# Kernel optimization log

Hardware: AMD Instinct MI355X
Metric: run time of the kernel (lower is better)

Reference implementation:

```python
import jax, jax.numpy as jnp
import numpy as np

MODEL_DIM = 1024
NUM_HEADS = 16
DEPTH = MODEL_DIM // NUM_HEADS


def setup_inputs() -> dict:
    key = jax.random.key(0)
    ks = jax.random.split(key, 9)
    B, S, D = 4, 2048, MODEL_DIM
    scale = 1.0 / np.sqrt(D)
    x = jax.random.normal(ks[0], (B, S, D), dtype=jnp.float32)
    wq = jax.random.normal(ks[1], (D, D), dtype=jnp.float32) * scale
    bq = jnp.zeros((D,), dtype=jnp.float32)
    wk = jax.random.normal(ks[2], (D, D), dtype=jnp.float32) * scale
    bk = jnp.zeros((D,), dtype=jnp.float32)
    wv = jax.random.normal(ks[3], (D, D), dtype=jnp.float32) * scale
    bv = jnp.zeros((D,), dtype=jnp.float32)
    wo = jax.random.normal(ks[4], (D, D), dtype=jnp.float32) * scale
    bo = jnp.zeros((D,), dtype=jnp.float32)
    return {"x": x, "wq": wq, "bq": bq, "wk": wk, "bk": bk,
            "wv": wv, "bv": bv, "wo": wo, "bo": bo}


def reference(x, wq, bq, wk, bk, wv, bv, wo, bo):
    B, S, D = x.shape
    H, dh = NUM_HEADS, DEPTH
    # projections
    q = (x @ wq + bq).reshape(B, S, H, dh).transpose(0, 2, 1, 3)  # [B,H,S,dh]
    k = (x @ wk + bk).reshape(B, S, H, dh).transpose(0, 2, 1, 3)
    v = (x @ wv + bv).reshape(B, S, H, dh).transpose(0, 2, 1, 3)
    # scaled dot-product attention (full score matrix, as in source)
    logits = jnp.einsum('bhqd,bhkd->bhqk', q, k) / jnp.sqrt(jnp.float32(dh))
    attn = jax.nn.softmax(logits, axis=-1)
    out = jnp.einsum('bhqk,bhkd->bhqd', attn, v)  # [B,H,S,dh]
    out = out.transpose(0, 2, 1, 3).reshape(B, S, D)
    return out @ wo + bo
```

## Files before the change

kernel.cpp:

```cpp
#include <hip/hip_runtime.h>
#include <hip/hip_bf16.h>


#define S_LEN 2048
#define DMODEL 1024
#define NH 16
#define DH 64
#define BATCH 4
#define MROWS (BATCH * S_LEN)
#define NELEM_X (MROWS * DMODEL)
#define NELEM_W (DMODEL * DMODEL)
#define NELEM_B DMODEL

typedef short short8 __attribute__((ext_vector_type(8)));
typedef float floatx4 __attribute__((ext_vector_type(4)));

__device__ __forceinline__ float bf2f(unsigned short u) {
    union { unsigned int i; float f; } c; c.i = ((unsigned int)u) << 16; return c.f;
}
__device__ __forceinline__ unsigned int f2bf_pk(float lo, float hi) {
    unsigned int r;
    asm("v_cvt_pk_bf16_f32 %0, %1, %2" : "=v"(r) : "v"(lo), "v"(hi));
    return r;
}
__device__ __forceinline__ void async_copy16(const void* g, void* l) {
    __builtin_amdgcn_global_load_lds(
        (const __attribute__((address_space(1))) unsigned int*)g,
        (__attribute__((address_space(3))) unsigned int*)l, 16, 0, 0);
}

__global__ void sniff_kernel(const unsigned short* __restrict__ x, int* flag) {
    __shared__ int cnt;
    if (threadIdx.x == 0) cnt = 0;
    __syncthreads();
    int c = 0;
    for (int i = threadIdx.x; i < 65536; i += 256) {
        unsigned int e = (x[i] >> 7) & 0xFFu;
        if (e >= 0xC0u) c++;
    }
    atomicAdd(&cnt, c);
    __syncthreads();
    if (threadIdx.x == 0) *flag = (cnt > 64) ? 1 : 0;
}

struct ConvArgs { const void* s[5]; unsigned short* d[5]; int n8[5]; };
__global__ void convert_all(ConvArgs a, const int* __restrict__ flag) {
    const int seg = blockIdx.y;
    const int f = *flag;
    const int n8 = a.n8[seg];
    unsigned short* dst = a.d[seg];
    int i = blockIdx.x * blockDim.x + threadIdx.x;
    const int stride = gridDim.x * blockDim.x;
    if (f) {
        const float4* s4 = (const float4*)a.s[seg];
        for (; i < n8; i += stride) {
            float4 x0 = s4[2 * i], x1 = s4[2 * i + 1];
            uint4 o;
            o.x = f2bf_pk(x0.x, x0.y); o.y = f2bf_pk(x0.z, x0.w);
            o.z = f2bf_pk(x1.x, x1.y); o.w = f2bf_pk(x1.z, x1.w);
            *(uint4*)(dst + (size_t)i * 8) = o;
        }
    } else {
        const uint4* s4 = (const uint4*)a.s[seg];
        for (; i < n8; i += stride) *(uint4*)(dst + (size_t)i * 8) = s4[i];
    }
}

struct TWArgs { const void* s[4]; unsigned short* d[4]; };
__global__ void transpose_w(TWArgs a, const int* __restrict__ flag) {
    __shared__ unsigned int Lt[64 * 33];
    const int z = blockIdx.z;
    const int f = *flag;
    const int k0 = blockIdx.x * 64, n0 = blockIdx.y * 64;
    const int t = threadIdx.x;
    const int c = t & 63, rgrp = t >> 6;

    if (f) {
        const float* W = (const float*)a.s[z];
        #pragma unroll
        for (int s = 0; s < 8; s++) {
            int r0 = rgrp * 16 + 2 * s;
            float v0 = W[(size_t)(k0 + r0) * DMODEL + n0 + c];
            float v1 = W[(size_t)(k0 + r0 + 1) * DMODEL + n0 + c];
            Lt[c * 33 + rgrp * 8 + s] = f2bf_pk(v0, v1);
        }
    } else {
        const unsigned short* W = (const unsigned short*)a.s[z];
        #pragma unroll
        for (int s = 0; s < 8; s++) {
            int r0 = rgrp * 16 + 2 * s;
            unsigned int lo = W[(size_t)(k0 + r0) * DMODEL + n0 + c];
            unsigned int hi = W[(size_t)(k0 + r0 + 1) * DMODEL + n0 + c];
            Lt[c * 33 + rgrp * 8 + s] = lo | (hi << 16);
        }
    }
    __syncthreads();
    const int row = t >> 2, j = t & 3;
    unsigned int* outp = (unsigned int*)(a.d[z] + (size_t)(n0 + row) * DMODEL + k0);
    #pragma unroll
    for (int i = 0; i < 8; i++) outp[j * 8 + i] = Lt[row * 33 + j * 8 + i];
}

__global__ __launch_bounds__(256, 2)
void gemm_bias_kernel(const unsigned short* __restrict__ X,
                      const unsigned short* __restrict__ T0, const unsigned short* __restrict__ B0, void* __restrict__ Y0,
                      const unsigned short* __restrict__ T1, const unsigned short* __restrict__ B1, void* __restrict__ Y1,
                      const unsigned short* __restrict__ T2, const unsigned short* __restrict__ B2, void* __restrict__ Y2,
                      float os0, float os1, float os2,
                      const int* __restrict__ flag, int fp32_out)
{
    const unsigned short* Wt = T0; const unsigned short* Bi = B0; void* Y = Y0;
    float os = os0;
    if (blockIdx.z == 1) { Wt = T1; Bi = B1; Y = Y1; os = os1; }
    else if (blockIdx.z == 2) { Wt = T2; Bi = B2; Y = Y2; os = os2; }
    const int f32o = fp32_out ? (*flag) : 0;

    __shared__ __align__(16) unsigned short As[128 * 32];
    __shared__ __align__(16) unsigned short Bs[128 * 32];

    const int t    = threadIdx.x;
    const int lane = t & 63;
    const int wid  = t >> 6;
    const int quad = lane >> 4;
    const int n16  = lane & 15;
    const int wm   = wid >> 1, wn = wid & 1;

    const int m0 = blockIdx.x * 128;
    const int n0 = blockIdx.y * 128;

    floatx4 acc[4][4];
    #pragma unroll
    for (int i = 0; i < 4; i++)
        #pragma unroll
        for (int j = 0; j < 4; j++) acc[i][j] = (floatx4){0.f, 0.f, 0.f, 0.f};

    const int r = t >> 2, c8 = (t & 3) * 8;

    for (int kb = 0; kb < DMODEL; kb += 32) {
        __syncthreads();
        async_copy16(X  + (size_t)(m0 + r)      * DMODEL + kb + c8, As + r * 32 + c8);
        async_copy16(X  + (size_t)(m0 + 64 + r) * DMODEL + kb + c8, As + (64 + r) * 32 + c8);
        async_copy16(Wt + (size_t)(n0 + r)      * DMODEL + kb + c8, Bs + r * 32 + c8);
        async_copy16(Wt + (size_t)(n0 + 64 + r) * DMODEL + kb + c8, Bs + (64 + r) * 32 + c8);
        __syncthreads();

        short8 af[4], bfr[4];
        #pragma unroll
        for (int mt = 0; mt < 4; mt++)
            af[mt] = *(const short8*)(As + (wm * 64 + mt * 16 + n16) * 32 + quad * 8);
        #pragma unroll
        for (int nt = 0; nt < 4; nt++)
            bfr[nt] = *(const short8*)(Bs + (wn * 64 + nt * 16 + n16) * 32 + quad * 8);
        #pragma unroll
        for (int mt = 0; mt < 4; mt++)
            #pragma unroll
            for (int nt = 0; nt < 4; nt++)
                acc[mt][nt] = __builtin_amdgcn_mfma_f32_16x16x32_bf16(af[mt], bfr[nt], acc[mt][nt], 0, 0, 0);
    }

    float bv4[4];
    #pragma unroll
    for (int nt = 0; nt < 4; nt++) bv4[nt] = bf2f(Bi[n0 + wn * 64 + nt * 16 + n16]) * os;
    #pragma unroll
    for (int mt = 0; mt < 4; mt++)
        #pragma unroll
        for (int rr = 0; rr < 4; rr++) {
            size_t row = (size_t)(m0 + wm * 64 + mt * 16 + quad * 4 + rr);
            if (f32o) {
                #pragma unroll
                for (int nt = 0; nt < 4; nt++) {
                    int col = n0 + wn * 64 + nt * 16 + n16;
                    ((float*)Y)[row * DMODEL + col] = fmaf(acc[mt][nt][rr], os, bv4[nt]);
                }
            } else {
                #pragma unroll
                for (int np = 0; np < 2; np++) {
                    float v0 = fmaf(acc[mt][2 * np    ][rr], os, bv4[2 * np]);
                    float v1 = fmaf(acc[mt][2 * np + 1][rr], os, bv4[2 * np + 1]);
                    unsigned int pk = f2bf_pk(v0, v1);
                    int col = n0 + wn * 64 + (2 * np) * 16 + n16;
                    ((unsigned short*)Y)[row * DMODEL + col]      = (unsigned short)pk;
                    ((unsigned short*)Y)[row * DMODEL + col + 16] = (unsigned short)(pk >> 16);
                }
            }
        }
}

__global__ __launch_bounds__(256, 4)
void attn_kernel(const unsigned short* Qw,
                 const unsigned short* __restrict__ Kw,
                 const unsigned short* __restrict__ Vw,
                 unsigned short* Ow)
{
    __shared__ __align__(16) unsigned short Ks[64 * 72];
    __shared__ __align__(16) unsigned short Vts[64 * 72];
    __shared__ __align__(16) unsigned short Ps[4 * 16 * 72];

    const int t    = threadIdx.x;
    const int lane = t & 63;
    const int w    = t >> 6;
    const int quad = lane >> 4;
    const int n16  = lane & 15;

    const int bid  = blockIdx.x;
    const int xs   = bid & 7;
    const int qblk = (bid >> 3) & 15;
    const int bh   = (bid >> 7) * 8 + xs;
    const int b    = bh >> 4;
    const int h    = bh & 15;

    const size_t baseRow = (size_t)b * S_LEN;
    const int hoff = h * DH;

    int qrow[2];
    short8 qf[2][2];
    #pragma unroll
    for (int g = 0; g < 2; g++) {
        qrow[g] = qblk * 128 + w * 32 + g * 16 + n16;
        qf[g][0] = *(const short8*)(Qw + (baseRow + qrow[g]) * DMODEL + hoff + quad * 8);
        qf[g][1] = *(const short8*)(Qw + (baseRow + qrow[g]) * DMODEL + hoff + 32 + quad * 8);
    }

    floatx4 acco[2][4];
    #pragma unroll
    for (int g = 0; g < 2; g++)
        #pragma unroll
        for (int i = 0; i < 4; i++) acco[g][i] = (floatx4){0.f, 0.f, 0.f, 0.f};
    float ls[2] = {0.f, 0.f};

    const int krow = t >> 3, kchk = (t & 7) * 8;
    const int vd = t & 63;

    for (int kb = 0; kb < S_LEN; kb += 64) {
        __syncthreads();
        *(float4*)(Ks + krow * 72 + kchk) =
            *(const float4*)(Kw + (baseRow + kb + krow) * DMODEL + hoff + kchk);
        *(float4*)(Ks + (krow + 32) * 72 + kchk) =
            *(const float4*)(Kw + (baseRow + kb + krow + 32) * DMODEL + hoff + kchk);
        #pragma unroll
        for (int rr = 0; rr < 4; rr++) {
            int kp0 = w * 8 + rr * 2;
            const unsigned short* vp = Vw + (baseRow + kb + 2 * kp0) * DMODEL + hoff + vd;
            unsigned int u0 = vp[0] | ((unsigned int)vp[DMODEL] << 16);
            unsigned int u1 = vp[2 * DMODEL] | ((unsigned int)vp[3 * DMODEL] << 16);
            *(uint2*)((unsigned int*)Vts + vd * 36 + kp0) = make_uint2(u0, u1);
        }
        __syncthreads();

        floatx4 sf[2][4];
        #pragma unroll
        for (int g = 0; g < 2; g++)
            #pragma unroll
            for (int kt = 0; kt < 4; kt++) sf[g][kt] = (floatx4){0.f, 0.f, 0.f, 0.f};
        #pragma unroll
        for (int kt = 0; kt < 4; kt++)
            #pragma unroll
            for (int ks = 0; ks < 2; ks++) {
                short8 kf = *(const short8*)(Ks + (kt * 16 + n16) * 72 + ks * 32 + quad * 8);
                sf[0][kt] = __builtin_amdgcn_mfma_f32_16x16x32_bf16(kf, qf[0][ks], sf[0][kt], 0, 0, 0);
                sf[1][kt] = __builtin_amdgcn_mfma_f32_16x16x32_bf16(kf, qf[1][ks], sf[1][kt], 0, 0, 0);
            }

        #pragma unroll
        for (int g = 0; g < 2; g++)
            #pragma unroll
            for (int kt = 0; kt < 4; kt++)
                #pragma unroll
                for (int rr = 0; rr < 4; rr++) {
                    float p = __builtin_exp2f(sf[g][kt][rr]);
                    sf[g][kt][rr] = p;
                    ls[g] += p;
                }

        unsigned short* Pw = Ps + w * 16 * 72;
        unsigned int*   Pu = (unsigned int*)Pw;
        short8 pf[2][2];
        #pragma unroll
        for (int g = 0; g < 2; g++) {
            #pragma unroll
            for (int kt = 0; kt < 4; kt++) {
                uint2 pk2 = make_uint2(f2bf_pk(sf[g][kt][0], sf[g][kt][1]),
                                       f2bf_pk(sf[g][kt][2], sf[g][kt][3]));
                *(uint2*)(Pu + n16 * 36 + kt * 8 + quad * 2) = pk2;
            }
            __asm__ volatile("" ::: "memory");
            #pragma unroll
            for (int ks = 0; ks < 2; ks++)
                pf[g][ks] = *(const short8*)(Pw + n16 * 72 + ks * 32 + quad * 8);
            __asm__ volatile("" ::: "memory");
        }

        #pragma unroll
        for (int ks = 0; ks < 2; ks++)
            #pragma unroll
            for (int dt = 0; dt < 4; dt++) {
                short8 vf = *(const short8*)(Vts + (dt * 16 + n16) * 72 + ks * 32 + quad * 8);
                acco[0][dt] = __builtin_amdgcn_mfma_f32_16x16x32_bf16(vf, pf[0][ks], acco[0][dt], 0, 0, 0);
                acco[1][dt] = __builtin_amdgcn_mfma_f32_16x16x32_bf16(vf, pf[1][ks], acco[1][dt], 0, 0, 0);
            }
    }

    #pragma unroll
    for (int g = 0; g < 2; g++) {
        float l = ls[g];
        l += __shfl_xor(l, 16);
        l += __shfl_xor(l, 32);
        const float rinv = 1.f / l;
        #pragma unroll
        for (int dt = 0; dt < 4; dt++) {
            uint2 o;
            o.x = f2bf_pk(acco[g][dt][0] * rinv, acco[g][dt][1] * rinv);
            o.y = f2bf_pk(acco[g][dt][2] * rinv, acco[g][dt][3] * rinv);
            *(uint2*)(Ow + (baseRow + qrow[g]) * DMODEL + hoff + dt * 16 + quad * 4) = o;
        }
    }
}

extern "C" void kernel_launch(void* const* d_in, const int* in_sizes, int n_in,
                              void* d_out, int out_size, void* d_ws, size_t ws_size,
                              hipStream_t stream)
{
    unsigned short* base = (unsigned short*)d_ws;
    int* flag = (int*)d_ws;
    unsigned short* xc  = base + 8;
    unsigned short* wqt = xc  + NELEM_X;
    unsigned short* wkt = wqt + NELEM_W;
    unsigned short* wvt = wkt + NELEM_W;
    unsigned short* wot = wvt + NELEM_W;
    unsigned short* bqc = wot + NELEM_W;
    unsigned short* bkc = bqc + NELEM_B;
    unsigned short* bvc = bkc + NELEM_B;
    unsigned short* boc = bvc + NELEM_B;
    unsigned short* qws = boc + NELEM_B;
    unsigned short* kws = qws + NELEM_X;
    unsigned short* vws = kws + NELEM_X;
    unsigned short* aws = qws;

    sniff_kernel<<<1, 256, 0, stream>>>((const unsigned short*)d_in[0], flag);

    ConvArgs ca;
    const void* csrc[5] = {d_in[0], d_in[2], d_in[4], d_in[6], d_in[8]};
    unsigned short* cdst[5] = {xc, bqc, bkc, bvc, boc};
    int cn8[5] = {NELEM_X / 8, NELEM_B / 8, NELEM_B / 8, NELEM_B / 8, NELEM_B / 8};
    for (int i = 0; i < 5; i++) { ca.s[i] = csrc[i]; ca.d[i] = cdst[i]; ca.n8[i] = cn8[i]; }
    convert_all<<<dim3(256, 5), 256, 0, stream>>>(ca, flag);

    TWArgs tw;
    const void* tsrc[4] = {d_in[1], d_in[3], d_in[5], d_in[7]};
    unsigned short* tdst[4] = {wqt, wkt, wvt, wot};
    for (int i = 0; i < 4; i++) { tw.s[i] = tsrc[i]; tw.d[i] = tdst[i]; }
    transpose_w<<<dim3(16, 16, 4), 256, 0, stream>>>(tw, flag);

    const float qscale = 0.125f * 1.44269504088896340736f;
    gemm_bias_kernel<<<dim3(64, 8, 3), 256, 0, stream>>>(
        xc, wqt, bqc, qws, wkt, bkc, kws, wvt, bvc, vws,
        qscale, 1.f, 1.f, flag, 0);

    attn_kernel<<<dim3(1024), 256, 0, stream>>>(qws, kws, vws, aws);

    gemm_bias_kernel<<<dim3(64, 8, 1), 256, 0, stream>>>(
        aws, wot, boc, d_out, wot, boc, d_out, wot, boc, d_out,
        1.f, 1.f, 1.f, flag, 1);
}
```

Baseline: 411.7 us.

## Pre-transpose V and enlarge attention query tile to 256 rows per block

Adds a separate kernel that writes V as [b,h,d,token] into the reused x workspace, so the attention kernel loads V tiles with vectorized 16-byte reads instead of scattered 2-byte gathers and in-loop packing. Each attention block now processes 256 query rows, four 16-row groups per wave, which halves the number of times K and V are streamed per head. The grid drops to 512 blocks, block indexing is simplified, and launch bounds are lowered to 2 for the larger register footprint. The costs are an extra kernel launch plus a V transpose round trip through memory, and reduced occupancy and parallelism.

Result: faster. 388.7 us (-5.6%).

```diff
diff --git a/kernel.cpp b/kernel.cpp
--- a/kernel.cpp
+++ b/kernel.cpp
@@ -101,6 +101,32 @@
     for (int i = 0; i < 8; i++) outp[j * 8 + i] = Lt[row * 33 + j * 8 + i];
 }
 
+__global__ void transpose_v(const unsigned short* __restrict__ vws,
+                            unsigned short* __restrict__ vt) {
+    __shared__ unsigned int Lt[64 * 33];
+    const int tok0 = blockIdx.x * 64;
+    const int bh   = blockIdx.y;
+    const int b    = bh >> 4;
+    const int h    = bh & 15;
+    const int t = threadIdx.x;
+    const int c = t & 63, rgrp = t >> 6;
+
+    const unsigned short* src = vws + (size_t)b * S_LEN * DMODEL + h * DH;
+    #pragma unroll
+    for (int s = 0; s < 8; s++) {
+        int r0 = rgrp * 16 + 2 * s;
+        unsigned int lo = src[(size_t)(tok0 + r0) * DMODEL + c];
+        unsigned int hi = src[(size_t)(tok0 + r0 + 1) * DMODEL + c];
+        Lt[c * 33 + rgrp * 8 + s] = lo | (hi << 16);
+    }
+    __syncthreads();
+    const int row = t >> 2, j = t & 3;
+    unsigned int* outp = (unsigned int*)(vt + (size_t)bh * DH * S_LEN
+                                            + (size_t)row * S_LEN + tok0);
+    #pragma unroll
+    for (int i = 0; i < 8; i++) outp[j * 8 + i] = Lt[row * 33 + j * 8 + i];
+}
+
 __global__ __launch_bounds__(256, 2)
 void gemm_bias_kernel(const unsigned short* __restrict__ X,
                       const unsigned short* __restrict__ T0, const unsigned short* __restrict__ B0, void* __restrict__ Y0,
@@ -186,10 +212,10 @@
         }
 }
 
-__global__ __launch_bounds__(256, 4)
+__global__ __launch_bounds__(256, 2)
 void attn_kernel(const unsigned short* Qw,
                  const unsigned short* __restrict__ Kw,
-                 const unsigned short* __restrict__ Vw,
+                 const unsigned short* __restrict__ VT,
                  unsigned short* Ow)
 {
     __shared__ __align__(16) unsigned short Ks[64 * 72];
@@ -203,33 +229,33 @@
     const int n16  = lane & 15;
 
     const int bid  = blockIdx.x;
-    const int xs   = bid & 7;
-    const int qblk = (bid >> 3) & 15;
-    const int bh   = (bid >> 7) * 8 + xs;
+    const int bh   = bid & 63;
+    const int qblk = bid >> 6;
     const int b    = bh >> 4;
     const int h    = bh & 15;
 
     const size_t baseRow = (size_t)b * S_LEN;
     const int hoff = h * DH;
-
-    int qrow[2];
-    short8 qf[2][2];
-    #pragma unroll
-    for (int g = 0; g < 2; g++) {
-        qrow[g] = qblk * 128 + w * 32 + g * 16 + n16;
+    const unsigned short* VTb = VT + (size_t)bh * DH * S_LEN;
+
+    int qrow[4];
+    short8 qf[4][2];
+    #pragma unroll
+    for (int g = 0; g < 4; g++) {
+        qrow[g] = qblk * 256 + w * 64 + g * 16 + n16;
         qf[g][0] = *(const short8*)(Qw + (baseRow + qrow[g]) * DMODEL + hoff + quad * 8);
         qf[g][1] = *(const short8*)(Qw + (baseRow + qrow[g]) * DMODEL + hoff + 32 + quad * 8);
     }
 
-    floatx4 acco[2][4];
-    #pragma unroll
-    for (int g = 0; g < 2; g++)
+    floatx4 acco[4][4];
+    #pragma unroll
+    for (int g = 0; g < 4; g++)
         #pragma unroll
         for (int i = 0; i < 4; i++) acco[g][i] = (floatx4){0.f, 0.f, 0.f, 0.f};
-    float ls[2] = {0.f, 0.f};
+    float ls[4] = {0.f, 0.f, 0.f, 0.f};
 
     const int krow = t >> 3, kchk = (t & 7) * 8;
-    const int vd = t & 63;
+    const int vrow = t >> 2, vchk = (t & 3) * 16;
 
     for (int kb = 0; kb < S_LEN; kb += 64) {
         __syncthreads();
@@ -237,19 +263,15 @@
             *(const float4*)(Kw + (baseRow + kb + krow) * DMODEL + hoff + kchk);
         *(float4*)(Ks + (krow + 32) * 72 + kchk) =
             *(const float4*)(Kw + (baseRow + kb + krow + 32) * DMODEL + hoff + kchk);
-        #pragma unroll
-        for (int rr = 0; rr < 4; rr++) {
-            int kp0 = w * 8 + rr * 2;
-            const unsigned short* vp = Vw + (baseRow + kb + 2 * kp0) * DMODEL + hoff + vd;
-            unsigned int u0 = vp[0] | ((unsigned int)vp[DMODEL] << 16);
-            unsigned int u1 = vp[2 * DMODEL] | ((unsigned int)vp[3 * DMODEL] << 16);
-            *(uint2*)((unsigned int*)Vts + vd * 36 + kp0) = make_uint2(u0, u1);
-        }
+        *(float4*)(Vts + vrow * 72 + vchk) =
+            *(const float4*)(VTb + (size_t)vrow * S_LEN + kb + vchk);
+        *(float4*)(Vts + vrow * 72 + vchk + 8) =
+            *(const float4*)(VTb + (size_t)vrow * S_LEN + kb + vchk + 8);
         __syncthreads();
 
-        floatx4 sf[2][4];
-        #pragma unroll
-        for (int g = 0; g < 2; g++)
+        floatx4 sf[4][4];
+        #pragma unroll
+        for (int g = 0; g < 4; g++)
             #pragma unroll
             for (int kt = 0; kt < 4; kt++) sf[g][kt] = (floatx4){0.f, 0.f, 0.f, 0.f};
         #pragma unroll
@@ -257,26 +279,26 @@
             #pragma unroll
             for (int ks = 0; ks < 2; ks++) {
                 short8 kf = *(const short8*)(Ks + (kt * 16 + n16) * 72 + ks * 32 + quad * 8);
-                sf[0][kt] = __builtin_amdgcn_mfma_f32_16x16x32_bf16(kf, qf[0][ks], sf[0][kt], 0, 0, 0);
-                sf[1][kt] = __builtin_amdgcn_mfma_f32_16x16x32_bf16(kf, qf[1][ks], sf[1][kt], 0, 0, 0);
+                #pragma unroll
+                for (int g = 0; g < 4; g++)
+                    sf[g][kt] = __builtin_amdgcn_mfma_f32_16x16x32_bf16(kf, qf[g][ks], sf[g][kt], 0, 0, 0);
             }
 
-        #pragma unroll
-        for (int g = 0; g < 2; g++)
+        unsigned short* Pw = Ps + w * 16 * 72;
+        unsigned int*   Pu = (unsigned int*)Pw;
+        short8 pf[4][2];
+        #pragma unroll
+        for (int g = 0; g < 4; g++) {
+            float lsum = 0.f;
             #pragma unroll
             for (int kt = 0; kt < 4; kt++)
                 #pragma unroll
                 for (int rr = 0; rr < 4; rr++) {
                     float p = __builtin_exp2f(sf[g][kt][rr]);
                     sf[g][kt][rr] = p;
-                    ls[g] += p;
+                    lsum += p;
                 }
-
-        unsigned short* Pw = Ps + w * 16 * 72;
-        unsigned int*   Pu = (unsigned int*)Pw;
-        short8 pf[2][2];
-        #pragma unroll
-        for (int g = 0; g < 2; g++) {
+            ls[g] += lsum;
             #pragma unroll
             for (int kt = 0; kt < 4; kt++) {
                 uint2 pk2 = make_uint2(f2bf_pk(sf[g][kt][0], sf[g][kt][1]),
@@ -284,9 +306,8 @@
                 *(uint2*)(Pu + n16 * 36 + kt * 8 + quad * 2) = pk2;
             }
             __asm__ volatile("" ::: "memory");
-            #pragma unroll
-            for (int ks = 0; ks < 2; ks++)
-                pf[g][ks] = *(const short8*)(Pw + n16 * 72 + ks * 32 + quad * 8);
+            pf[g][0] = *(const short8*)(Pw + n16 * 72 + quad * 8);
+            pf[g][1] = *(const short8*)(Pw + n16 * 72 + 32 + quad * 8);
             __asm__ volatile("" ::: "memory");
         }
 
@@ -295,13 +316,14 @@
             #pragma unroll
             for (int dt = 0; dt < 4; dt++) {
                 short8 vf = *(const short8*)(Vts + (dt * 16 + n16) * 72 + ks * 32 + quad * 8);
-                acco[0][dt] = __builtin_amdgcn_mfma_f32_16x16x32_bf16(vf, pf[0][ks], acco[0][dt], 0, 0, 0);
-                acco[1][dt] = __builtin_amdgcn_mfma_f32_16x16x32_bf16(vf, pf[1][ks], acco[1][dt], 0, 0, 0);
+                #pragma unroll
+                for (int g = 0; g < 4; g++)
+                    acco[g][dt] = __builtin_amdgcn_mfma_f32_16x16x32_bf16(vf, pf[g][ks], acco[g][dt], 0, 0, 0);
             }
     }
 
     #pragma unroll
-    for (int g = 0; g < 2; g++) {
+    for (int g = 0; g < 4; g++) {
         float l = ls[g];
         l += __shfl_xor(l, 16);
         l += __shfl_xor(l, 32);
@@ -335,6 +357,7 @@
     unsigned short* kws = qws + NELEM_X;
     unsigned short* vws = kws + NELEM_X;
     unsigned short* aws = qws;
+    unsigned short* vtw = xc;
 
     sniff_kernel<<<1, 256, 0, stream>>>((const unsigned short*)d_in[0], flag);
 
@@ -356,7 +379,9 @@
         xc, wqt, bqc, qws, wkt, bkc, kws, wvt, bvc, vws,
         qscale, 1.f, 1.f, flag, 0);
 
-    attn_kernel<<<dim3(1024), 256, 0, stream>>>(qws, kws, vws, aws);
+    transpose_v<<<dim3(32, 64), 256, 0, stream>>>(vws, vtw);
+
+    attn_kernel<<<dim3(512), 256, 0, stream>>>(qws, kws, vtw, aws);
 
     gemm_bias_kernel<<<dim3(64, 8, 1), 256, 0, stream>>>(
         aws, wot, boc, d_out, wot, boc, d_out, wot, boc, d_out,
```
